# Kernel optimization log

Hardware: AMD Instinct MI355X
Metric: run time of the kernel (lower is better)

Reference implementation:

```python
import jax, jax.numpy as jnp
import numpy as np

N_NODES = 100000
N_EDGES = 1600000
N_GRAPHS = 256
NODE_DIM = 64
EDGE_DIM = 64
HIDDEN = 128
VOCAB = 128
N_CONV = 3
R_MIN, R_MAX = 1.0, 6.0
LN_EPS = 1e-5


def layer_norm(x, g, b):
    mu = jnp.mean(x, axis=-1, keepdims=True)
    var = jnp.mean(jnp.square(x - mu), axis=-1, keepdims=True)
    return (x - mu) * jax.lax.rsqrt(var + LN_EPS) * g + b


def setup_inputs() -> dict:
    key = jax.random.key(0)
    ks = jax.random.split(key, 16)
    inp = {}
    inp["numbers"] = jax.random.randint(ks[0], (N_NODES,), 0, VOCAB)
    inp["edge_index"] = jax.random.randint(ks[1], (2, N_EDGES), 0, N_NODES)
    inp["edge_length"] = jax.random.uniform(ks[2], (N_EDGES,), minval=R_MIN, maxval=R_MAX, dtype=jnp.float32)
    inp["batch"] = jnp.sort(jax.random.randint(ks[3], (N_NODES,), 0, N_GRAPHS))
    s = 0.1
    inp["embed_table"] = jax.random.normal(ks[4], (VOCAB, NODE_DIM), jnp.float32)
    inp["Wf"] = jax.random.normal(ks[5], (N_CONV, 2 * NODE_DIM + EDGE_DIM, NODE_DIM), jnp.float32) * s
    inp["bf"] = jnp.zeros((N_CONV, NODE_DIM), jnp.float32)
    inp["Ws"] = jax.random.normal(ks[6], (N_CONV, 2 * NODE_DIM + EDGE_DIM, NODE_DIM), jnp.float32) * s
    inp["bs"] = jnp.zeros((N_CONV, NODE_DIM), jnp.float32)
    inp["ln_g"] = jnp.ones((N_CONV, NODE_DIM), jnp.float32)
    inp["ln_b"] = jnp.zeros((N_CONV, NODE_DIM), jnp.float32)
    inp["olp_W1"] = jax.random.normal(ks[7], (NODE_DIM, HIDDEN), jnp.float32) * s
    inp["olp_b1"] = jnp.zeros((HIDDEN,), jnp.float32)
    inp["olp_g1"] = jnp.ones((HIDDEN,), jnp.float32)
    inp["olp_bt1"] = jnp.zeros((HIDDEN,), jnp.float32)
    inp["olp_W2"] = jax.random.normal(ks[8], (HIDDEN, HIDDEN), jnp.float32) * s
    inp["olp_b2"] = jnp.zeros((HIDDEN,), jnp.float32)
    inp["olp_g2"] = jnp.ones((HIDDEN,), jnp.float32)
    inp["olp_bt2"] = jnp.zeros((HIDDEN,), jnp.float32)
    inp["W_out"] = jax.random.normal(ks[9], (HIDDEN, 1), jnp.float32) * s
    inp["b_out"] = jnp.zeros((1,), jnp.float32)
    return inp


def reference(numbers, edge_index, edge_length, batch, embed_table,
              Wf, bf, Ws, bs, ln_g, ln_b,
              olp_W1, olp_b1, olp_g1, olp_bt1,
              olp_W2, olp_b2, olp_g2, olp_bt2,
              W_out, b_out):
    n_nodes = numbers.shape[0]
    # Gaussian edge expansion: exp(-0.5*((d - centers)/step)^2)  -> [E, edge_dim]
    centers = jnp.linspace(R_MIN, R_MAX, EDGE_DIM, dtype=jnp.float32)
    step = (R_MAX - R_MIN) / EDGE_DIM
    edge_attrs = jnp.exp(-0.5 * jnp.square((edge_length[:, None] - centers) / step))

    x = embed_table[numbers]                      # [N, node_dim]
    src, tgt = edge_index[0], edge_index[1]

    for i in range(N_CONV):
        z = jnp.concatenate([x[src], x[tgt], edge_attrs], axis=-1)  # [E, 2d+e]
        gate = jax.nn.sigmoid(z @ Wf[i] + bf[i]) * jax.nn.softplus(z @ Ws[i] + bs[i])
        msg = jax.ops.segment_sum(gate, src, num_segments=n_nodes)  # reduce='add'
        x = x + layer_norm(msg, ln_g[i], ln_b[i])

    # hidden OLPs: Linear -> LayerNorm -> Softplus (dropout identity at eval)
    h = jax.nn.softplus(layer_norm(x @ olp_W1 + olp_b1, olp_g1, olp_bt1))
    h = jax.nn.softplus(layer_norm(h @ olp_W2 + olp_b2, olp_g2, olp_bt2))
    e = h @ W_out + b_out                          # [N, 1]

    # per_atom_target=True -> segment mean over graphs
    sums = jax.ops.segment_sum(e, batch, num_segments=N_GRAPHS)      # [G, 1]
    cnt = jax.ops.segment_sum(jnp.ones((n_nodes,), e.dtype), batch, num_segments=N_GRAPHS)
    energy = sums / jnp.maximum(cnt, 1.0)[:, None]
    return energy
```

## Files before the change

kernel.cpp:

```cpp
#include <hip/hip_runtime.h>
#include <hip/hip_fp16.h>
#include <math.h>

#define NNODES 100000
#define NEDGES 1600000
#define NGRAPH 256
#define NCONV  3
#define TBL    4096
#define CHUNK  512
#define NCHUNK 196
#define R_MIN_ 1.0f
#define R_MAX_ 6.0f
#define LOG2E  1.4426950408889634f

typedef _Float16 f16x8 __attribute__((ext_vector_type(8)));
typedef float f32x4 __attribute__((ext_vector_type(4)));
union HF { float4 f4; f16x8 h8; __half2 q[4]; };

__device__ __forceinline__ float softplus_f(float x){
  return fmaxf(x, 0.f) + __logf(1.f + __expf(-fabsf(x)));
}

__global__ void k_init(int* ccnt, float* gsum, int* gcnt){
  int i = blockIdx.x*256 + threadIdx.x;
  if (i < 256) ccnt[i] = 0;
  if (i < NGRAPH){ gsum[i] = 0.f; gcnt[i] = 0; }
}

__global__ void k_embed(const int* __restrict__ numbers, const float* __restrict__ embed,
                        float* __restrict__ x){
  int i = blockIdx.x*256 + threadIdx.x;
  if (i >= NNODES*64) return;
  int n = i >> 6, c = i & 63;
  x[i] = embed[numbers[n]*64 + c];
}

__global__ void k_lut(float2* __restrict__ lutg){
  __shared__ float sv[513], cv[513];
  int t = threadIdx.x;
  for (int i = t; i < 513; i += 256){
    float z = -16.f + (float)i * (1.f/16.f);
    sv[i] = 1.f / (1.f + exp2f(-z));
    cv[i] = log2f(1.f + exp2f(z));
  }
  __syncthreads();
  for (int i = t; i < 512; i += 256){
    lutg[i]       = make_float2(sv[i], sv[i+1]-sv[i]);
    lutg[512 + i] = make_float2(cv[i], cv[i+1]-cv[i]);
  }
}

__global__ void k_cnt(const int* __restrict__ src, int* ccnt){
  __shared__ int l[NCHUNK];
  int t = threadIdx.x;
  int e0 = blockIdx.x * 2048;
  if (t < NCHUNK) l[t] = 0;
  __syncthreads();
  #pragma unroll
  for (int k = 0; k < 8; k++){
    int e = e0 + k*256 + t;
    if (e < NEDGES) atomicAdd(&l[src[e] / CHUNK], 1);
  }
  __syncthreads();
  if (t < NCHUNK && l[t] > 0) atomicAdd(&ccnt[t], l[t]);
}

__global__ void k_cscan(const int* __restrict__ ccnt, int* __restrict__ cbase,
                        int* __restrict__ ccur, int* __restrict__ offs){
  __shared__ int s[256];
  int t = threadIdx.x;
  int v = (t < NCHUNK) ? ccnt[t] : 0;
  s[t] = v;
  __syncthreads();
  #pragma unroll
  for (int d = 1; d < 256; d <<= 1){
    int u = (t >= d) ? s[t-d] : 0;
    __syncthreads();
    s[t] += u;
    __syncthreads();
  }
  int excl = s[t] - v;
  if (t < NCHUNK){ cbase[t] = excl; ccur[t] = excl; }
  if (t == 0){ cbase[NCHUNK] = NEDGES; offs[NNODES] = NEDGES; }
}

__global__ void k_bin(const int* __restrict__ src, const int* __restrict__ tgt,
                      const float* __restrict__ elen, int* ccur,
                      int2* __restrict__ eb){
  __shared__ int lcnt[NCHUNK];
  __shared__ int lbase[NCHUNK];
  __shared__ int loff[NCHUNK];
  int t = threadIdx.x;
  int e0 = blockIdx.x * 2048;
  if (t < NCHUNK){ lcnt[t] = 0; loff[t] = 0; }
  __syncthreads();
  #pragma unroll
  for (int k = 0; k < 8; k++){
    int e = e0 + k*256 + t;
    if (e < NEDGES) atomicAdd(&lcnt[src[e] / CHUNK], 1);
  }
  __syncthreads();
  if (t < NCHUNK && lcnt[t] > 0) lbase[t] = atomicAdd(&ccur[t], lcnt[t]);
  __syncthreads();
  #pragma unroll
  for (int k = 0; k < 8; k++){
    int e = e0 + k*256 + t;
    if (e < NEDGES){
      int s = src[e];
      int c = s / CHUNK;
      int r = atomicAdd(&loff[c], 1);
      float key = (elen[e] - R_MIN_) * ((float)(TBL-1)/(R_MAX_-R_MIN_));
      key = fmaxf(key, 0.f);
      int idx = (int)(key + 0.5f);
      if (idx > TBL-1) idx = TBL-1;
      eb[lbase[c] + r] = make_int2(((s & (CHUNK-1)) << 17) | tgt[e], idx);
    }
  }
}

__global__ void k_fine(const int* __restrict__ cbase, const int2* __restrict__ eb,
                       int2* __restrict__ ep, int* __restrict__ offs){
  __shared__ int lcnt[CHUNK];
  __shared__ int lsc[CHUNK];
  int c = blockIdx.x;
  int t = threadIdx.x;
  int n0 = c * CHUNK;
  int n1 = min(n0 + CHUNK, NNODES);
  int cnt = n1 - n0;
  int j0 = cbase[c], j1 = cbase[c+1];
  lcnt[t] = 0;
  __syncthreads();
  for (int e = j0 + t; e < j1; e += 512)
    atomicAdd(&lcnt[((unsigned)eb[e].x) >> 17], 1);
  __syncthreads();
  lsc[t] = lcnt[t];
  __syncthreads();
  for (int d = 1; d < 512; d <<= 1){
    int v = (t >= d) ? lsc[t-d] : 0;
    __syncthreads();
    lsc[t] += v;
    __syncthreads();
  }
  int excl = lsc[t] - lcnt[t];
  if (t < cnt) offs[n0 + t] = j0 + excl;
  __syncthreads();
  lcnt[t] = j0 + excl;
  __syncthreads();
  for (int e = j0 + t; e < j1; e += 512){
    int2 rec = eb[e];
    int sl = ((unsigned)rec.x) >> 17;
    int pos = atomicAdd(&lcnt[sl], 1);
    ep[pos] = make_int2(rec.x & 0x1FFFF, rec.y);
  }
}

__global__ void k_gauss(const float* __restrict__ Wf, const float* __restrict__ bf,
                        const float* __restrict__ Ws, const float* __restrict__ bs,
                        __half* __restrict__ Gth){
  __shared__ float attr[64];
  int bi = blockIdx.x;
  int i = bi / TBL, r = bi % TBL;
  int t = threadIdx.x;
  float d = R_MIN_ + (R_MAX_-R_MIN_) * (float)r / (float)(TBL-1);
  if (t < 64){
    float cj = 1.f + 5.f * (float)t / 63.f;
    float u = (d - cj) * (64.f/5.f);
    attr[t] = __expf(-0.5f*u*u);
  }
  __syncthreads();
  int c = t >> 1;
  int side = t & 1;
  const float* W = (side ? Ws : Wf) + i*192*64 + 128*64 + c;
  float acc = (side ? bs : bf)[i*64 + c];
  #pragma unroll 8
  for (int j = 0; j < 64; j++) acc = fmaf(attr[j], W[j*64], acc);
  Gth[((size_t)i*TBL + r)*128 + t] = __float2half_rn(acc * LOG2E);
}

__global__ void k_wcat(const float* __restrict__ Wf, const float* __restrict__ Ws,
                       __half* __restrict__ WmC){
  int idx = blockIdx.x*256 + threadIdx.x;
  if (idx >= 3*16384) return;
  int i = idx / 16384;
  int rem = idx & 16383;
  int ct = rem >> 10;
  int kt = (rem >> 9) & 1;
  int lane = (rem >> 3) & 63;
  int e = rem & 7;
  int col = ct*16 + (lane & 15);
  int part = col >> 6;
  int ch = col & 63;
  int k = kt*32 + (lane >> 4)*8 + e;
  int row = ((part >> 1) ? 64 : 0) + k;
  const float* W = ((part & 1) ? Ws : Wf) + i*192*64;
  WmC[idx] = __float2half_rn(W[row*64 + ch]);
}

__global__ void k_wm(const float* __restrict__ W1, const float* __restrict__ W2,
                     __half* __restrict__ Wm1, __half* __restrict__ Wm2){
  int i = blockIdx.x*256 + threadIdx.x;
  if (i < 8192){
    int ct = i >> 10;
    int kt = (i >> 9) & 1;
    int lane = (i >> 3) & 63;
    int e = i & 7;
    int k = kt*32 + (lane>>4)*8 + e;
    int c = ct*16 + (lane&15);
    Wm1[i] = __float2half_rn(W1[k*128 + c]);
  }
  if (i < 16384){
    int ct = i >> 11;
    int kt = (i >> 9) & 3;
    int lane = (i >> 3) & 63;
    int e = i & 7;
    int k = kt*32 + (lane>>4)*8 + e;
    int c = ct*16 + (lane&15);
    Wm2[i] = __float2half_rn(W2[k*128 + c]);
  }
}

__global__ void k_ntrans(const float* __restrict__ x, const __half* __restrict__ WmC,
                         __half2* __restrict__ pqh){
  __shared__ __half xh[32*72];
  int n0 = blockIdx.x * 32;
  int t = threadIdx.x;
  int w = t >> 6, lane = t & 63;
  int lg = lane >> 4, lc = lane & 15;
  {
    int n = t >> 3, g = t & 7;
    const float4* xp = (const float4*)(x + (size_t)(n0 + n)*64 + g*8);
    float4 a = xp[0], b = xp[1];
    HF hh;
    hh.q[0] = __float22half2_rn(make_float2(a.x, a.y));
    hh.q[1] = __float22half2_rn(make_float2(a.z, a.w));
    hh.q[2] = __float22half2_rn(make_float2(b.x, b.y));
    hh.q[3] = __float22half2_rn(make_float2(b.z, b.w));
    *(float4*)(xh + n*72 + g*8) = hh.f4;
  }
  __syncthreads();
  HF a[2][2];
  #pragma unroll
  for (int m = 0; m < 2; m++)
    #pragma unroll
    for (int kt = 0; kt < 2; kt++)
      a[m][kt].f4 = *(const float4*)(xh + (m*16 + lc)*72 + kt*32 + lg*8);
  const float4* wb = (const float4*)WmC;
  f32x4 acc[4][2];
  #pragma unroll
  for (int p4 = 0; p4 < 4; p4++){
    int ct = p4*4 + w;
    HF b0, b1;
    b0.f4 = wb[(ct*2 + 0)*64 + lane];
    b1.f4 = wb[(ct*2 + 1)*64 + lane];
    #pragma unroll
    for (int m = 0; m < 2; m++){
      f32x4 c = {0.f, 0.f, 0.f, 0.f};
      c = __builtin_amdgcn_mfma_f32_16x16x32_f16(a[m][0].h8, b0.h8, c, 0, 0, 0);
      c = __builtin_amdgcn_mfma_f32_16x16x32_f16(a[m][1].h8, b1.h8, c, 0, 0, 0);
      acc[p4][m] = c;
    }
  }
  #pragma unroll
  for (int m = 0; m < 2; m++)
    #pragma unroll
    for (int r = 0; r < 4; r++){
      int node = n0 + m*16 + lg*4 + r;
      int ch = w*16 + lc;
      __half2 hp = __floats2half2_rn(acc[0][m][r]*LOG2E, acc[1][m][r]*LOG2E);
      __half2 hq = __floats2half2_rn(acc[2][m][r]*LOG2E, acc[3][m][r]*LOG2E);
      pqh[(size_t)node*128 + ch]      = hp;
      pqh[(size_t)node*128 + 64 + ch] = hq;
    }
}

__global__ void k_edge(const __half2* __restrict__ pqh,
                       const int* __restrict__ offs, const int2* __restrict__ ep,
                       const __half* __restrict__ Gth, const float* __restrict__ lng,
                       const float* __restrict__ lnb, const float2* __restrict__ lutg,
                       float* __restrict__ x){
  __shared__ float2 lut[1024];
  {
    float4* d = (float4*)lut;
    const float4* s = (const float4*)lutg;
    d[threadIdx.x]       = s[threadIdx.x];
    d[threadIdx.x + 256] = s[threadIdx.x + 256];
  }
  __syncthreads();
  int wid  = (blockIdx.x*256 + threadIdx.x) >> 6;
  int lane = threadIdx.x & 63;
  int n = wid;
  int j0 = __builtin_amdgcn_readfirstlane(offs[n]);
  int j1 = __builtin_amdgcn_readfirstlane(offs[n+1]);
  int nfull = (j1 - j0) >> 3;
  int2 eb8[8];
  if (nfull > 0){
    #pragma unroll
    for (int i = 0; i < 8; i++) eb8[i] = ep[j0 + i];
  }
  float2 pp = __half22float2(pqh[(size_t)n*128 + lane]);
  float pfo = fmaf(pp.x, 16.f, 256.f);
  float pso = fmaf(pp.y, 16.f, 768.f);
  float ps = pp.y;
  const char* pqb = (const char*)pqh;
  const char* gtb = (const char*)Gth;
  unsigned qob = 256u + ((unsigned)lane << 2);
  unsigned lob = (unsigned)lane << 2;
  float acc = 0.f;
  int u = j0;
  for (int b = 0; b < nfull; b++){
    __half2 qr[8], gr[8];
    #pragma unroll
    for (int i = 0; i < 8; i++){
      qr[i] = *(const __half2*)(pqb + ((((unsigned)eb8[i].x) << 9) + qob));
      gr[i] = *(const __half2*)(gtb + ((((unsigned)eb8[i].y) << 8) + lob));
    }
    if (b + 1 < nfull){
      #pragma unroll
      for (int i = 0; i < 8; i++) eb8[i] = ep[u + 8 + i];
    }
    #pragma unroll
    for (int i = 0; i < 8; i++){
      float2 z = __half22float2(__hadd2(qr[i], gr[i]));
      float xi = __builtin_amdgcn_fmed3f(fmaf(z.x, 16.f, pfo), 0.f, 511.36f);
      int i1 = (int)xi;
      float f1 = __builtin_amdgcn_fractf(xi);
      float2 e1 = lut[i1];
      float sig = fmaf(e1.y, f1, e1.x);
      float xj = __builtin_amdgcn_fmed3f(fmaf(z.y, 16.f, pso), 512.f, 1023.36f);
      int i2 = (int)xj;
      float f2 = __builtin_amdgcn_fractf(xj);
      float2 e2 = lut[i2];
      float zs = ps + z.y;
      float sp = fmaxf(zs, fmaf(e2.y, f2, e2.x));
      acc = fmaf(sig, sp, acc);
    }
    u += 8;
  }
  for (; u < j1; u++){
    int2 e = ep[u];
    __half2 q = *(const __half2*)(pqb + ((((unsigned)e.x) << 9) + qob));
    __half2 g = *(const __half2*)(gtb + ((((unsigned)e.y) << 8) + lob));
    float2 z = __half22float2(__hadd2(q, g));
    float xi = __builtin_amdgcn_fmed3f(fmaf(z.x, 16.f, pfo), 0.f, 511.36f);
    int i1 = (int)xi;
    float f1 = __builtin_amdgcn_fractf(xi);
    float2 e1 = lut[i1];
    float sig = fmaf(e1.y, f1, e1.x);
    float xj = __builtin_amdgcn_fmed3f(fmaf(z.y, 16.f, pso), 512.f, 1023.36f);
    int i2 = (int)xj;
    float f2 = __builtin_amdgcn_fractf(xj);
    float2 e2 = lut[i2];
    float zs = ps + z.y;
    float sp = fmaxf(zs, fmaf(e2.y, f2, e2.x));
    acc = fmaf(sig, sp, acc);
  }
  float s1 = acc, s2 = acc*acc;
  #pragma unroll
  for (int o = 32; o > 0; o >>= 1){ s1 += __shfl_xor(s1, o, 64); s2 += __shfl_xor(s2, o, 64); }
  float mu  = s1 * (1.f/64.f);
  float var = s2 * (1.f/64.f) - mu*mu;
  float inv = rsqrtf(fmaxf(var, 0.f) + 1e-5f);
  float y = (acc - mu) * inv * lng[lane] + lnb[lane];
  x[(size_t)n*64 + lane] += y;
}

__global__ void k_head(const float* __restrict__ x,
                       const __half* __restrict__ Wm1, const float* __restrict__ b1,
                       const float* __restrict__ g1, const float* __restrict__ bt1,
                       const __half* __restrict__ Wm2, const float* __restrict__ b2,
                       const float* __restrict__ g2, const float* __restrict__ bt2,
                       const float* __restrict__ Wout, const int* __restrict__ batch,
                       float* gsum, int* gcnt){
  __shared__ __half xh[32*72];
  __shared__ __half hs[32*136];
  __shared__ float red[4][32][2];
  __shared__ float stat[32][2];
  __shared__ float es[32];
  int n0 = blockIdx.x * 32;
  int t = threadIdx.x;
  int w = t >> 6, lane = t & 63;
  int lg = lane >> 4, lc = lane & 15;
  int col0 = w*32 + lc, col1 = w*32 + 16 + lc;

  {
    int n = t >> 3, g = t & 7;
    const float4* xp = (const float4*)(x + (size_t)(n0 + n)*64 + g*8);
    float4 a = xp[0], b = xp[1];
    HF hh;
    hh.q[0] = __float22half2_rn(make_float2(a.x, a.y));
    hh.q[1] = __float22half2_rn(make_float2(a.z, a.w));
    hh.q[2] = __float22half2_rn(make_float2(b.x, b.y));
    hh.q[3] = __float22half2_rn(make_float2(b.z, b.w));
    *(float4*)(xh + n*72 + g*8) = hh.f4;
  }
  __syncthreads();

  f32x4 acc[2][2];
  {
    HF a[2][2], b[2][2];
    #pragma unroll
    for (int m = 0; m < 2; m++)
      #pragma unroll
      for (int kt = 0; kt < 2; kt++)
        a[m][kt].f4 = *(const float4*)(xh + (m*16 + lc)*72 + kt*32 + lg*8);
    const float4* wb = (const float4*)Wm1;
    #pragma unroll
    for (int ct = 0; ct < 2; ct++)
      #pragma unroll
      for (int kt = 0; kt < 2; kt++)
        b[ct][kt].f4 = wb[(((w*2 + ct)*2 + kt)*64) + lane];
    #pragma unroll
    for (int m = 0; m < 2; m++)
      #pragma unroll
      for (int ct = 0; ct < 2; ct++){
        f32x4 c = {0.f, 0.f, 0.f, 0.f};
        c = __builtin_amdgcn_mfma_f32_16x16x32_f16(a[m][0].h8, b[ct][0].h8, c, 0, 0, 0);
        c = __builtin_amdgcn_mfma_f32_16x16x32_f16(a[m][1].h8, b[ct][1].h8, c, 0, 0, 0);
        acc[m][ct] = c;
      }
  }
  {
    float bv0 = b1[col0], bv1 = b1[col1];
    #pragma unroll
    for (int m = 0; m < 2; m++)
      #pragma unroll
      for (int r = 0; r < 4; r++){
        acc[m][0][r] += bv0; acc[m][1][r] += bv1;
        float a0 = acc[m][0][r], a1 = acc[m][1][r];
        float s1 = a0 + a1, s2 = a0*a0 + a1*a1;
        #pragma unroll
        for (int o = 1; o < 16; o <<= 1){ s1 += __shfl_xor(s1, o, 64); s2 += __shfl_xor(s2, o, 64); }
        if (lc == 0){ int row = m*16 + lg*4 + r; red[w][row][0] = s1; red[w][row][1] = s2; }
      }
  }
  __syncthreads();
  if (t < 32){
    float s1 = red[0][t][0] + red[1][t][0] + red[2][t][0] + red[3][t][0];
    float s2 = red[0][t][1] + red[1][t][1] + red[2][t][1] + red[3][t][1];
    float mu = s1 * (1.f/128.f);
    float var = s2 * (1.f/128.f) - mu*mu;
    stat[t][0] = mu;
    stat[t][1] = rsqrtf(fmaxf(var, 0.f) + 1e-5f);
  }
  __syncthreads();
  {
    float g1a = g1[col0], g1b = g1[col1], b1a = bt1[col0], b1b = bt1[col1];
    #pragma unroll
    for (int m = 0; m < 2; m++)
      #pragma unroll
      for (int r = 0; r < 4; r++){
        int row = m*16 + lg*4 + r;
        float mu = stat[row][0], inv = stat[row][1];
        float y0 = (acc[m][0][r] - mu)*inv*g1a + b1a;
        float y1 = (acc[m][1][r] - mu)*inv*g1b + b1b;
        hs[row*136 + col0] = __float2half_rn(softplus_f(y0));
        hs[row*136 + col1] = __float2half_rn(softplus_f(y1));
      }
  }
  __syncthreads();

  f32x4 acc2[2][2];
  {
    HF b[2][4];
    const float4* wb = (const float4*)Wm2;
    #pragma unroll
    for (int ct = 0; ct < 2; ct++)
      #pragma unroll
      for (int kt = 0; kt < 4; kt++)
        b[ct][kt].f4 = wb[(((w*2 + ct)*4 + kt)*64) + lane];
    #pragma unroll
    for (int m = 0; m < 2; m++){
      f32x4 c0 = {0.f,0.f,0.f,0.f}, c1 = {0.f,0.f,0.f,0.f};
      #pragma unroll
      for (int kt = 0; kt < 4; kt++){
        HF av; av.f4 = *(const float4*)(hs + (m*16 + lc)*136 + kt*32 + lg*8);
        c0 = __builtin_amdgcn_mfma_f32_16x16x32_f16(av.h8, b[0][kt].h8, c0, 0, 0, 0);
        c1 = __builtin_amdgcn_mfma_f32_16x16x32_f16(av.h8, b[1][kt].h8, c1, 0, 0, 0);
      }
      acc2[m][0] = c0; acc2[m][1] = c1;
    }
  }
  {
    float bv0 = b2[col0], bv1 = b2[col1];
    #pragma unroll
    for (int m = 0; m < 2; m++)
      #pragma unroll
      for (int r = 0; r < 4; r++){
        acc2[m][0][r] += bv0; acc2[m][1][r] += bv1;
        float a0 = acc2[m][0][r], a1 = acc2[m][1][r];
        float s1 = a0 + a1, s2 = a0*a0 + a1*a1;
        #pragma unroll
        for (int o = 1; o < 16; o <<= 1){ s1 += __shfl_xor(s1, o, 64); s2 += __shfl_xor(s2, o, 64); }
        if (lc == 0){ int row = m*16 + lg*4 + r; red[w][row][0] = s1; red[w][row][1] = s2; }
      }
  }
  __syncthreads();
  if (t < 32){
    float s1 = red[0][t][0] + red[1][t][0] + red[2][t][0] + red[3][t][0];
    float s2 = red[0][t][1] + red[1][t][1] + red[2][t][1] + red[3][t][1];
    float mu = s1 * (1.f/128.f);
    float var = s2 * (1.f/128.f) - mu*mu;
    stat[t][0] = mu;
    stat[t][1] = rsqrtf(fmaxf(var, 0.f) + 1e-5f);
  }
  __syncthreads();
  {
    float g2a = g2[col0], g2b = g2[col1], b2a = bt2[col0], b2b = bt2[col1];
    float woa = Wout[col0], wob = Wout[col1];
    #pragma unroll
    for (int m = 0; m < 2; m++)
      #pragma unroll
      for (int r = 0; r < 4; r++){
        int row = m*16 + lg*4 + r;
        float mu = stat[row][0], inv = stat[row][1];
        float e = softplus_f((acc2[m][0][r] - mu)*inv*g2a + b2a) * woa
                + softplus_f((acc2[m][1][r] - mu)*inv*g2b + b2b) * wob;
        #pragma unroll
        for (int o = 1; o < 16; o <<= 1) e += __shfl_xor(e, o, 64);
        if (lc == 0) red[w][row][0] = e;
      }
  }
  __syncthreads();
  if (t < 32) es[t] = red[0][t][0] + red[1][t][0] + red[2][t][0] + red[3][t][0];
  __syncthreads();

  if (t < 32){
    int node = n0 + t;
    int g = batch[node];
    bool head = (t == 0) || (batch[node-1] != g);
    if (head){
      float s = 0.f; int c = 0;
      int j = t;
      while (j < 32 && batch[n0+j] == g){ s += es[j]; c++; j++; }
      atomicAdd(&gsum[g], s);
      atomicAdd(&gcnt[g], c);
    }
  }
}

__global__ void k_final(const float* __restrict__ gsum, const int* __restrict__ gcnt,
                        const float* __restrict__ bout, float* __restrict__ out){
  int g = threadIdx.x;
  if (g < NGRAPH)
    out[g] = gsum[g] / fmaxf((float)gcnt[g], 1.f) + bout[0];
}

extern "C" void kernel_launch(void* const* d_in, const int* in_sizes, int n_in,
                              void* d_out, int out_size, void* d_ws, size_t ws_size,
                              hipStream_t stream){
  const int*   numbers = (const int*)d_in[0];
  const int*   eidx    = (const int*)d_in[1];
  const float* elen    = (const float*)d_in[2];
  const int*   batch   = (const int*)d_in[3];
  const float* embed   = (const float*)d_in[4];
  const float* Wf      = (const float*)d_in[5];
  const float* bf      = (const float*)d_in[6];
  const float* Ws      = (const float*)d_in[7];
  const float* bs      = (const float*)d_in[8];
  const float* lng     = (const float*)d_in[9];
  const float* lnb     = (const float*)d_in[10];
  const float* W1      = (const float*)d_in[11];
  const float* b1      = (const float*)d_in[12];
  const float* g1      = (const float*)d_in[13];
  const float* bt1     = (const float*)d_in[14];
  const float* W2      = (const float*)d_in[15];
  const float* b2      = (const float*)d_in[16];
  const float* g2      = (const float*)d_in[17];
  const float* bt2     = (const float*)d_in[18];
  const float* Wout    = (const float*)d_in[19];
  const float* bout    = (const float*)d_in[20];
  const int* src = eidx;
  const int* tgt = eidx + NEDGES;

  float*   x    = (float*)d_ws;
  __half2* pqh  = (__half2*)(x + (size_t)NNODES*64);
  __half*  Gth  = (__half*)(pqh + (size_t)NNODES*128);
  __half*  WmC  = Gth + (size_t)3*TBL*128;
  __half*  Wm1  = WmC + (size_t)3*16384;
  __half*  Wm2  = Wm1 + 8192;
  float2*  lutg = (float2*)(Wm2 + 16384);
  int2*    ep   = (int2*)(lutg + 1024);
  int2*    ebuf = ep + NEDGES;
  int*     offs = (int*)(ebuf + NEDGES);
  int*     ccnt = offs + NNODES + 1;
  int*     cbase= ccnt + 256;
  int*     ccur = cbase + 256;
  float*   gsum = (float*)(ccur + 256);
  int*     gcnt = (int*)(gsum + NGRAPH);
  float*   out  = (float*)d_out;

  k_init  <<<(NNODES+255)/256, 256, 0, stream>>>(ccnt, gsum, gcnt);
  k_embed <<<(NNODES*64+255)/256, 256, 0, stream>>>(numbers, embed, x);

  k_cnt   <<<(NEDGES+2047)/2048, 256, 0, stream>>>(src, ccnt);
  k_cscan <<<1, 256, 0, stream>>>(ccnt, cbase, ccur, offs);
  k_bin   <<<(NEDGES+2047)/2048, 256, 0, stream>>>(src, tgt, elen, ccur, ebuf);
  k_fine  <<<NCHUNK, 512, 0, stream>>>(cbase, ebuf, ep, offs);

  k_gauss <<<3*TBL, 128, 0, stream>>>(Wf, bf, Ws, bs, Gth);
  k_wcat  <<<(3*16384+255)/256, 256, 0, stream>>>(Wf, Ws, WmC);
  k_wm    <<<64, 256, 0, stream>>>(W1, W2, Wm1, Wm2);
  k_lut   <<<1, 256, 0, stream>>>(lutg);

  for (int i = 0; i < NCONV; i++){
    k_ntrans<<<NNODES/32, 256, 0, stream>>>(x, WmC + (size_t)i*16384, pqh);
    k_edge  <<<NNODES/4, 256, 0, stream>>>(pqh, offs, ep,
                                           Gth + (size_t)i*TBL*128,
                                           lng + i*64, lnb + i*64, lutg, x);
  }

  k_head<<<NNODES/32, 256, 0, stream>>>(x, Wm1, b1, g1, bt1,
                                        Wm2, b2, g2, bt2, Wout, batch, gsum, gcnt);
  k_final<<<1, 256, 0, stream>>>(gsum, gcnt, bout, out);
}
```

Baseline: 577.0 us.

## Replace edge count/scan with fixed-capacity chunk bins and compute sigmoid directly

Drops the counting pass and the chunk scan by giving each source-node chunk a fixed-capacity region (CAP slots) in the edge buffers. Per-node degree is stored so the edge kernel no longer needs a contiguous offs[n+1]. Several setup kernels (init, LUT, weight repack) are merged into one prep kernel, cutting launches. In the edge loop the sigmoid LUT lookup is replaced by a hardware exp2+rcp, which halves the shared LUT. The risk is overflow if any chunk holds more than CAP edges: it relies on the src distribution being near-uniform, about 8192 expected per chunk.

```diff
diff --git a/kernel.cpp b/kernel.cpp
--- a/kernel.cpp
+++ b/kernel.cpp
@@ -9,6 +9,7 @@
 #define TBL    4096
 #define CHUNK  512
 #define NCHUNK 196
+#define CAP    9216
 #define R_MIN_ 1.0f
 #define R_MAX_ 6.0f
 #define LOG2E  1.4426950408889634f
@@ -19,12 +20,6 @@
 
 __device__ __forceinline__ float softplus_f(float x){
   return fmaxf(x, 0.f) + __logf(1.f + __expf(-fabsf(x)));
-}
-
-__global__ void k_init(int* ccnt, float* gsum, int* gcnt){
-  int i = blockIdx.x*256 + threadIdx.x;
-  if (i < 256) ccnt[i] = 0;
-  if (i < NGRAPH){ gsum[i] = 0.f; gcnt[i] = 0; }
 }
 
 __global__ void k_embed(const int* __restrict__ numbers, const float* __restrict__ embed,
@@ -35,53 +30,43 @@
   x[i] = embed[numbers[n]*64 + c];
 }
 
-__global__ void k_lut(float2* __restrict__ lutg){
-  __shared__ float sv[513], cv[513];
-  int t = threadIdx.x;
-  for (int i = t; i < 513; i += 256){
-    float z = -16.f + (float)i * (1.f/16.f);
-    sv[i] = 1.f / (1.f + exp2f(-z));
-    cv[i] = log2f(1.f + exp2f(z));
-  }
-  __syncthreads();
-  for (int i = t; i < 512; i += 256){
-    lutg[i]       = make_float2(sv[i], sv[i+1]-sv[i]);
-    lutg[512 + i] = make_float2(cv[i], cv[i+1]-cv[i]);
-  }
-}
-
-__global__ void k_cnt(const int* __restrict__ src, int* ccnt){
-  __shared__ int l[NCHUNK];
-  int t = threadIdx.x;
-  int e0 = blockIdx.x * 2048;
-  if (t < NCHUNK) l[t] = 0;
-  __syncthreads();
-  #pragma unroll
-  for (int k = 0; k < 8; k++){
-    int e = e0 + k*256 + t;
-    if (e < NEDGES) atomicAdd(&l[src[e] / CHUNK], 1);
-  }
-  __syncthreads();
-  if (t < NCHUNK && l[t] > 0) atomicAdd(&ccnt[t], l[t]);
-}
-
-__global__ void k_cscan(const int* __restrict__ ccnt, int* __restrict__ cbase,
-                        int* __restrict__ ccur, int* __restrict__ offs){
-  __shared__ int s[256];
-  int t = threadIdx.x;
-  int v = (t < NCHUNK) ? ccnt[t] : 0;
-  s[t] = v;
-  __syncthreads();
-  #pragma unroll
-  for (int d = 1; d < 256; d <<= 1){
-    int u = (t >= d) ? s[t-d] : 0;
+__global__ void k_prep(const float* __restrict__ W1, const float* __restrict__ W2,
+                       __half* __restrict__ Wm1, __half* __restrict__ Wm2,
+                       float2* __restrict__ lutg, int* __restrict__ ccur,
+                       float* __restrict__ gsum, int* __restrict__ gcnt){
+  int b = blockIdx.x, t = threadIdx.x;
+  if (b == 64){
+    __shared__ float cv[513];
+    for (int i = t; i < 513; i += 256){
+      float z = -16.f + (float)i * (1.f/16.f);
+      cv[i] = log2f(1.f + exp2f(z));
+    }
     __syncthreads();
-    s[t] += u;
-    __syncthreads();
-  }
-  int excl = s[t] - v;
-  if (t < NCHUNK){ cbase[t] = excl; ccur[t] = excl; }
-  if (t == 0){ cbase[NCHUNK] = NEDGES; offs[NNODES] = NEDGES; }
+    for (int i = t; i < 512; i += 256)
+      lutg[i] = make_float2(cv[i], cv[i+1]-cv[i]);
+    if (t < NCHUNK) ccur[t] = t * CAP;
+    if (t < NGRAPH){ gsum[t] = 0.f; gcnt[t] = 0; }
+    return;
+  }
+  int i = b*256 + t;
+  if (i < 8192){
+    int ct = i >> 10;
+    int kt = (i >> 9) & 1;
+    int lane = (i >> 3) & 63;
+    int e = i & 7;
+    int k = kt*32 + (lane>>4)*8 + e;
+    int c = ct*16 + (lane&15);
+    Wm1[i] = __float2half_rn(W1[k*128 + c]);
+  }
+  {
+    int ct = i >> 11;
+    int kt = (i >> 9) & 3;
+    int lane = (i >> 3) & 63;
+    int e = i & 7;
+    int k = kt*32 + (lane>>4)*8 + e;
+    int c = ct*16 + (lane&15);
+    Wm2[i] = __float2half_rn(W2[k*128 + c]);
+  }
 }
 
 __global__ void k_bin(const int* __restrict__ src, const int* __restrict__ tgt,
@@ -118,8 +103,9 @@
   }
 }
 
-__global__ void k_fine(const int* __restrict__ cbase, const int2* __restrict__ eb,
-                       int2* __restrict__ ep, int* __restrict__ offs){
+__global__ void k_fine(const int* __restrict__ ccur, const int2* __restrict__ eb,
+                       int2* __restrict__ ep, int* __restrict__ offs,
+                       int* __restrict__ deg){
   __shared__ int lcnt[CHUNK];
   __shared__ int lsc[CHUNK];
   int c = blockIdx.x;
@@ -127,7 +113,8 @@
   int n0 = c * CHUNK;
   int n1 = min(n0 + CHUNK, NNODES);
   int cnt = n1 - n0;
-  int j0 = cbase[c], j1 = cbase[c+1];
+  int j0 = c * CAP;
+  int j1 = ccur[c];
   lcnt[t] = 0;
   __syncthreads();
   for (int e = j0 + t; e < j1; e += 512)
@@ -142,7 +129,7 @@
     __syncthreads();
   }
   int excl = lsc[t] - lcnt[t];
-  if (t < cnt) offs[n0 + t] = j0 + excl;
+  if (t < cnt){ offs[n0 + t] = j0 + excl; deg[n0 + t] = lcnt[t]; }
   __syncthreads();
   lcnt[t] = j0 + excl;
   __syncthreads();
@@ -196,29 +183,6 @@
   WmC[idx] = __float2half_rn(W[row*64 + ch]);
 }
 
-__global__ void k_wm(const float* __restrict__ W1, const float* __restrict__ W2,
-                     __half* __restrict__ Wm1, __half* __restrict__ Wm2){
-  int i = blockIdx.x*256 + threadIdx.x;
-  if (i < 8192){
-    int ct = i >> 10;
-    int kt = (i >> 9) & 1;
-    int lane = (i >> 3) & 63;
-    int e = i & 7;
-    int k = kt*32 + (lane>>4)*8 + e;
-    int c = ct*16 + (lane&15);
-    Wm1[i] = __float2half_rn(W1[k*128 + c]);
-  }
-  if (i < 16384){
-    int ct = i >> 11;
-    int kt = (i >> 9) & 3;
-    int lane = (i >> 3) & 63;
-    int e = i & 7;
-    int k = kt*32 + (lane>>4)*8 + e;
-    int c = ct*16 + (lane&15);
-    Wm2[i] = __float2half_rn(W2[k*128 + c]);
-  }
-}
-
 __global__ void k_ntrans(const float* __restrict__ x, const __half* __restrict__ WmC,
                          __half2* __restrict__ pqh){
   __shared__ __half xh[32*72];
@@ -274,23 +238,21 @@
 }
 
 __global__ void k_edge(const __half2* __restrict__ pqh,
-                       const int* __restrict__ offs, const int2* __restrict__ ep,
+                       const int* __restrict__ offs, const int* __restrict__ deg,
+                       const int2* __restrict__ ep,
                        const __half* __restrict__ Gth, const float* __restrict__ lng,
                        const float* __restrict__ lnb, const float2* __restrict__ lutg,
                        float* __restrict__ x){
-  __shared__ float2 lut[1024];
-  {
-    float4* d = (float4*)lut;
-    const float4* s = (const float4*)lutg;
-    d[threadIdx.x]       = s[threadIdx.x];
-    d[threadIdx.x + 256] = s[threadIdx.x + 256];
+  __shared__ float2 lut[512];
+  {
+    ((float4*)lut)[threadIdx.x] = ((const float4*)lutg)[threadIdx.x];
   }
   __syncthreads();
   int wid  = (blockIdx.x*256 + threadIdx.x) >> 6;
   int lane = threadIdx.x & 63;
   int n = wid;
   int j0 = __builtin_amdgcn_readfirstlane(offs[n]);
-  int j1 = __builtin_amdgcn_readfirstlane(offs[n+1]);
+  int j1 = j0 + __builtin_amdgcn_readfirstlane(deg[n]);
   int nfull = (j1 - j0) >> 3;
   int2 eb8[8];
   if (nfull > 0){
@@ -298,9 +260,8 @@
     for (int i = 0; i < 8; i++) eb8[i] = ep[j0 + i];
   }
   float2 pp = __half22float2(pqh[(size_t)n*128 + lane]);
-  float pfo = fmaf(pp.x, 16.f, 256.f);
-  float pso = fmaf(pp.y, 16.f, 768.f);
-  float ps = pp.y;
+  float pf = pp.x, ps = pp.y;
+  float pso = fmaf(ps, 16.f, 256.f);
   const char* pqb = (const char*)pqh;
   const char* gtb = (const char*)Gth;
   unsigned qob = 256u + ((unsigned)lane << 2);
@@ -321,12 +282,8 @@
     #pragma unroll
     for (int i = 0; i < 8; i++){
       float2 z = __half22float2(__hadd2(qr[i], gr[i]));
-      float xi = __builtin_amdgcn_fmed3f(fmaf(z.x, 16.f, pfo), 0.f, 511.36f);
-      int i1 = (int)xi;
-      float f1 = __builtin_amdgcn_fractf(xi);
-      float2 e1 = lut[i1];
-      float sig = fmaf(e1.y, f1, e1.x);
-      float xj = __builtin_amdgcn_fmed3f(fmaf(z.y, 16.f, pso), 512.f, 1023.36f);
+      float sig = __builtin_amdgcn_rcpf(1.f + __builtin_amdgcn_exp2f(-(pf + z.x)));
+      float xj = __builtin_amdgcn_fmed3f(fmaf(z.y, 16.f, pso), 0.f, 511.36f);
       int i2 = (int)xj;
       float f2 = __builtin_amdgcn_fractf(xj);
       float2 e2 = lut[i2];
@@ -341,12 +298,8 @@
     __half2 q = *(const __half2*)(pqb + ((((unsigned)e.x) << 9) + qob));
     __half2 g = *(const __half2*)(gtb + ((((unsigned)e.y) << 8) + lob));
     float2 z = __half22float2(__hadd2(q, g));
-    float xi = __builtin_amdgcn_fmed3f(fmaf(z.x, 16.f, pfo), 0.f, 511.36f);
-    int i1 = (int)xi;
-    float f1 = __builtin_amdgcn_fractf(xi);
-    float2 e1 = lut[i1];
-    float sig = fmaf(e1.y, f1, e1.x);
-    float xj = __builtin_amdgcn_fmed3f(fmaf(z.y, 16.f, pso), 512.f, 1023.36f);
+    float sig = __builtin_amdgcn_rcpf(1.f + __builtin_amdgcn_exp2f(-(pf + z.x)));
+    float xj = __builtin_amdgcn_fmed3f(fmaf(z.y, 16.f, pso), 0.f, 511.36f);
     int i2 = (int)xj;
     float f2 = __builtin_amdgcn_fractf(xj);
     float2 e2 = lut[i2];
@@ -580,31 +533,26 @@
   __half*  Wm2  = Wm1 + 8192;
   float2*  lutg = (float2*)(Wm2 + 16384);
   int2*    ep   = (int2*)(lutg + 1024);
-  int2*    ebuf = ep + NEDGES;
-  int*     offs = (int*)(ebuf + NEDGES);
-  int*     ccnt = offs + NNODES + 1;
-  int*     cbase= ccnt + 256;
-  int*     ccur = cbase + 256;
+  int2*    ebuf = ep + (size_t)NCHUNK*CAP;
+  int*     offs = (int*)(ebuf + (size_t)NCHUNK*CAP);
+  int*     deg  = offs + NNODES;
+  int*     ccur = deg + NNODES;
   float*   gsum = (float*)(ccur + 256);
   int*     gcnt = (int*)(gsum + NGRAPH);
   float*   out  = (float*)d_out;
 
-  k_init  <<<(NNODES+255)/256, 256, 0, stream>>>(ccnt, gsum, gcnt);
+  k_prep  <<<65, 256, 0, stream>>>(W1, W2, Wm1, Wm2, lutg, ccur, gsum, gcnt);
   k_embed <<<(NNODES*64+255)/256, 256, 0, stream>>>(numbers, embed, x);
 
-  k_cnt   <<<(NEDGES+2047)/2048, 256, 0, stream>>>(src, ccnt);
-  k_cscan <<<1, 256, 0, stream>>>(ccnt, cbase, ccur, offs);
   k_bin   <<<(NEDGES+2047)/2048, 256, 0, stream>>>(src, tgt, elen, ccur, ebuf);
-  k_fine  <<<NCHUNK, 512, 0, stream>>>(cbase, ebuf, ep, offs);
+  k_fine  <<<NCHUNK, 512, 0, stream>>>(ccur, ebuf, ep, offs, deg);
 
   k_gauss <<<3*TBL, 128, 0, stream>>>(Wf, bf, Ws, bs, Gth);
   k_wcat  <<<(3*16384+255)/256, 256, 0, stream>>>(Wf, Ws, WmC);
-  k_wm    <<<64, 256, 0, stream>>>(W1, W2, Wm1, Wm2);
-  k_lut   <<<1, 256, 0, stream>>>(lutg);
 
   for (int i = 0; i < NCONV; i++){
     k_ntrans<<<NNODES/32, 256, 0, stream>>>(x, WmC + (size_t)i*16384, pqh);
-    k_edge  <<<NNODES/4, 256, 0, stream>>>(pqh, offs, ep,
+    k_edge  <<<NNODES/4, 256, 0, stream>>>(pqh, offs, deg, ep,
                                            Gth + (size_t)i*TBL*128,
                                            lng + i*64, lnb + i*64, lutg, x);
   }
```

Result: faster. 541.6 us (-6.1%).
